# Optimization experiments

Measured on AMD Instinct MI355X. Metric: run time of the kernel, lower is better.

Reference implementation:

```python
import jax, jax.numpy as jnp
import numpy as np
import math

PHI = (1.0 + math.sqrt(5.0)) / 2.0
LUT_SIZE = 4096
D_MODEL = 2048
BATCH = 8192
TWO_PI = 2.0 * math.pi


def lut_sin_cos(theta, sin_table, cos_table):
    """LUT-based sin/cos with linear interpolation over [0, 2*pi)."""
    n = sin_table.shape[0]
    pos = jnp.mod(theta, TWO_PI) * (n / TWO_PI)        # [B, D] in [0, n)
    i0f = jnp.floor(pos)
    frac = pos - i0f
    i0 = i0f.astype(jnp.int32) % n
    i1 = (i0 + 1) % n
    s = sin_table[i0] * (1.0 - frac) + sin_table[i1] * frac
    c = cos_table[i0] * (1.0 - frac) + cos_table[i1] * frac
    return s, c


def setup_inputs() -> dict:
    key = jax.random.key(0)
    ks = jax.random.split(key, 6)
    x_real = jax.random.normal(ks[0], (BATCH, D_MODEL), dtype=jnp.float32)
    x_imag = jax.random.normal(ks[1], (BATCH, D_MODEL), dtype=jnp.float32)
    t = jax.random.uniform(ks[2], (BATCH,), dtype=jnp.float32)
    memory_real = jnp.zeros((BATCH, D_MODEL), dtype=jnp.float32)
    memory_imag = jnp.zeros((BATCH, D_MODEL), dtype=jnp.float32)
    w_trigger = jax.random.normal(ks[3], (D_MODEL,), dtype=jnp.float32) * 0.02
    b_trigger = jnp.zeros((D_MODEL,), dtype=jnp.float32)
    w_state = jax.random.normal(ks[4], (D_MODEL,), dtype=jnp.float32) * 0.02
    b_state = jnp.zeros((D_MODEL,), dtype=jnp.float32)
    k = jnp.asarray(3.0, dtype=jnp.float32)
    grid = jnp.arange(LUT_SIZE, dtype=jnp.float32) * (TWO_PI / LUT_SIZE)
    sin_table = jnp.sin(grid)
    cos_table = jnp.cos(grid)
    return dict(x_real=x_real, x_imag=x_imag, t=t,
                memory_real=memory_real, memory_imag=memory_imag,
                w_trigger=w_trigger, b_trigger=b_trigger,
                w_state=w_state, b_state=b_state, k=k,
                sin_table=sin_table, cos_table=cos_table)


def reference(x_real, x_imag, t, memory_real, memory_imag,
              w_trigger, b_trigger, w_state, b_state, k,
              sin_table, cos_table):
    scale = math.sqrt(x_real.shape[-1])
    t_phi = t[:, None] * PHI                                  # [B, 1]

    # trigger phase
    wl_trigger = 1.0 + jnp.abs(w_trigger)
    theta_tr = x_real / wl_trigger + b_trigger + t_phi
    theta_ti = x_imag / wl_trigger + b_trigger + t_phi
    sin_tr, cos_tr = lut_sin_cos(theta_tr, sin_table, cos_table)
    sin_ti, cos_ti = lut_sin_cos(theta_ti, sin_table, cos_table)
    trigger_real = cos_tr * cos_ti - sin_tr * sin_ti
    trigger_imag = cos_tr * sin_ti + sin_tr * cos_ti

    # interference -> exponential decay gate
    interference_raw = jnp.sum(trigger_real * x_real + trigger_imag * x_imag, axis=-1)
    interference_clamped = jnp.clip(interference_raw / scale, -1.0, 1.0)
    x_inv = (1.0 - interference_clamped) / 2.0
    k_eff = jnp.abs(k) + 0.1
    alpha = jnp.exp(-k_eff * x_inv)[:, None]                  # [B, 1]

    # blend with (detached) memory, then re-evolve
    blended_real = alpha * x_real + (1.0 - alpha) * memory_real
    blended_imag = alpha * x_imag + (1.0 - alpha) * memory_imag
    wl_state = 1.0 + jnp.abs(w_state)
    theta_sr = blended_real / wl_state + b_state + t_phi
    theta_si = blended_imag / wl_state + b_state + t_phi
    sin_sr, cos_sr = lut_sin_cos(theta_sr, sin_table, cos_table)
    sin_si, cos_si = lut_sin_cos(theta_si, sin_table, cos_table)
    evolved_real = cos_sr * cos_si - sin_sr * sin_si
    evolved_imag = cos_sr * sin_si + sin_sr * cos_si
    return evolved_real, evolved_imag
```

## Files before the change

### kernel.cpp

```cpp
#include <hip/hip_runtime.h>

#define DMODEL   2048
#define NTHREADS 256
#define ROWS_PER_BLK 4
#define CHUNKS   8

typedef float fx4 __attribute__((ext_vector_type(4)));

__device__ __forceinline__ void fast_sincos(float theta, float& s, float& c) {
    const float INV_TWO_PI = 0.15915494309189535f;
    float r  = theta * INV_TWO_PI;
    float rr = r - floorf(r);
#if __has_builtin(__builtin_amdgcn_sinf) && __has_builtin(__builtin_amdgcn_cosf)
    s = __builtin_amdgcn_sinf(rr);
    c = __builtin_amdgcn_cosf(rr);
#else
    s = __sinf(rr * 6.283185307179586f);
    c = __cosf(rr * 6.283185307179586f);
#endif
}

__device__ __forceinline__ float fast_rcp(float x) {
#if __has_builtin(__builtin_amdgcn_rcpf)
    return __builtin_amdgcn_rcpf(x);
#else
    return 1.0f / x;
#endif
}

template <typename T>
__device__ __forceinline__ void nt_store(T v, T* p) {
#if __has_builtin(__builtin_nontemporal_store)
    __builtin_nontemporal_store(v, p);
#else
    *p = v;
#endif
}

__global__ __launch_bounds__(NTHREADS, 4)
void liquid_echo_kernel(const float* __restrict__ x_real,
                        const float* __restrict__ x_imag,
                        const float* __restrict__ tvec,
                        const float* __restrict__ memory_real,
                        const float* __restrict__ memory_imag,
                        const float* __restrict__ w_trigger,
                        const float* __restrict__ b_trigger,
                        const float* __restrict__ w_state,
                        const float* __restrict__ b_state,
                        const float* __restrict__ kptr,
                        float* __restrict__ out,
                        int nrows,
                        size_t imag_off)
{
    const int lane = threadIdx.x & 63;
    const int row  = blockIdx.x * ROWS_PER_BLK + (threadIdx.x >> 6);
    if (row >= nrows) return;

    const float t_phi = tvec[row] * 1.6180339887498948f;
    const size_t rb   = (size_t)row * DMODEL;
    const int cbase   = lane << 2;

    fx4 xr[CHUNKS], xi[CHUNKS];
    #pragma unroll
    for (int k = 0; k < CHUNKS; ++k) {
        const int c = (k << 8) + cbase;
        xr[k] = *(const fx4*)(x_real + rb + c);
        xi[k] = *(const fx4*)(x_imag + rb + c);
    }

    float sxy[CHUNKS * 4];
    float partial = 0.0f;
    #pragma unroll
    for (int k = 0; k < CHUNKS; ++k) {
        const int c = (k << 8) + cbase;
        const fx4 wt = *(const fx4*)(w_trigger + c);
        const fx4 bt = *(const fx4*)(b_trigger + c);
        #pragma unroll
        for (int j = 0; j < 4; ++j) {
            float iw   = fast_rcp(1.0f + fabsf(wt[j]));
            float base = bt[j] + t_phi;
            float sx   = xr[k][j] + xi[k][j];
            sxy[k * 4 + j] = sx;
            float ths  = fmaf(sx, iw, base + base);
            float s, cc;
            fast_sincos(ths, s, cc);
            partial = fmaf(cc, xr[k][j], partial);
            partial = fmaf(s,  xi[k][j], partial);
        }
    }

    fx4 mr[CHUNKS], mi[CHUNKS];
    #pragma unroll
    for (int k = 0; k < CHUNKS; ++k) {
        const int c = (k << 8) + cbase;
        mr[k] = *(const fx4*)(memory_real + rb + c);
        mi[k] = *(const fx4*)(memory_imag + rb + c);
    }

    #pragma unroll
    for (int off = 32; off > 0; off >>= 1)
        partial += __shfl_xor(partial, off, 64);

    float ic    = partial * (1.0f / 45.254833995939045f);
    ic          = fminf(1.0f, fmaxf(-1.0f, ic));
    float x_inv = (1.0f - ic) * 0.5f;
    float k_eff = fabsf(kptr[0]) + 0.1f;
    const float alpha = __expf(-k_eff * x_inv);
    const float oma   = 1.0f - alpha;

    float* outr = out + rb;
    float* outi = out + imag_off + rb;

    #pragma unroll
    for (int k = 0; k < CHUNKS; ++k) {
        const int c = (k << 8) + cbase;
        const fx4 ws = *(const fx4*)(w_state + c);
        const fx4 bs = *(const fx4*)(b_state + c);
        fx4 er, ei;
        #pragma unroll
        for (int j = 0; j < 4; ++j) {
            float smm  = mr[k][j] + mi[k][j];
            float sb   = fmaf(alpha, sxy[k * 4 + j], oma * smm);
            float iw   = fast_rcp(1.0f + fabsf(ws[j]));
            float base = bs[j] + t_phi;
            float ths  = fmaf(sb, iw, base + base);
            float s, cc;
            fast_sincos(ths, s, cc);
            er[j] = cc;
            ei[j] = s;
        }
        nt_store(er, (fx4*)(outr + c));
        nt_store(ei, (fx4*)(outi + c));
    }
}

extern "C" void kernel_launch(void* const* d_in, const int* in_sizes, int n_in,
                              void* d_out, int out_size, void* d_ws, size_t ws_size,
                              hipStream_t stream) {
    const float* x_real      = (const float*)d_in[0];
    const float* x_imag      = (const float*)d_in[1];
    const float* t           = (const float*)d_in[2];
    const float* memory_real = (const float*)d_in[3];
    const float* memory_imag = (const float*)d_in[4];
    const float* w_trigger   = (const float*)d_in[5];
    const float* b_trigger   = (const float*)d_in[6];
    const float* w_state     = (const float*)d_in[7];
    const float* b_state     = (const float*)d_in[8];
    const float* k           = (const float*)d_in[9];
    float* out = (float*)d_out;

    int B = in_sizes[0] / DMODEL;
    size_t imag_off = (size_t)out_size / 2;
    int grid = (B + ROWS_PER_BLK - 1) / ROWS_PER_BLK;

    liquid_echo_kernel<<<grid, NTHREADS, 0, stream>>>(
        x_real, x_imag, t, memory_real, memory_imag,
        w_trigger, b_trigger, w_state, b_state, k,
        out, B, imag_off);
}
```

Measured before the change: 346.2 us.

## Split into interference-reduction kernel and grid-stride double-buffered evolve kernel

```diff
diff --git a/kernel.cpp b/kernel.cpp
--- a/kernel.cpp
+++ b/kernel.cpp
@@ -1,11 +1,16 @@
 #include <hip/hip_runtime.h>
 
-#define DMODEL   2048
-#define NTHREADS 256
-#define ROWS_PER_BLK 4
-#define CHUNKS   8
+#define DMODEL    2048
+#define F4ROW     (DMODEL / 4)
+#define ROWSHIFT  9
+#define NTHREADS  256
+#define WPB       (NTHREADS / 64)
+#define MAXBLK    2048
+#define MAXROWS_STATIC 16384
 
 typedef float fx4 __attribute__((ext_vector_type(4)));
+
+__device__ float g_rowsum[MAXROWS_STATIC];
 
 __device__ __forceinline__ void fast_sincos(float theta, float& s, float& c) {
     const float INV_TWO_PI = 0.15915494309189535f;
@@ -37,101 +42,139 @@
 #endif
 }
 
-__global__ __launch_bounds__(NTHREADS, 4)
-void liquid_echo_kernel(const float* __restrict__ x_real,
-                        const float* __restrict__ x_imag,
-                        const float* __restrict__ tvec,
-                        const float* __restrict__ memory_real,
-                        const float* __restrict__ memory_imag,
-                        const float* __restrict__ w_trigger,
-                        const float* __restrict__ b_trigger,
-                        const float* __restrict__ w_state,
-                        const float* __restrict__ b_state,
-                        const float* __restrict__ kptr,
-                        float* __restrict__ out,
-                        int nrows,
-                        size_t imag_off)
+__global__ __launch_bounds__(NTHREADS)
+void k1_interference(const float* __restrict__ x_real,
+                     const float* __restrict__ x_imag,
+                     const float* __restrict__ tvec,
+                     const float* __restrict__ w_trigger,
+                     const float* __restrict__ b_trigger,
+                     float* __restrict__ rowsum_ext,
+                     int use_ext,
+                     int nrows)
 {
     const int lane = threadIdx.x & 63;
-    const int row  = blockIdx.x * ROWS_PER_BLK + (threadIdx.x >> 6);
+    const int row  = blockIdx.x * WPB + (threadIdx.x >> 6);
     if (row >= nrows) return;
 
+    float* __restrict__ rowsum = use_ext ? rowsum_ext : g_rowsum;
+
     const float t_phi = tvec[row] * 1.6180339887498948f;
-    const size_t rb   = (size_t)row * DMODEL;
-    const int cbase   = lane << 2;
-
-    fx4 xr[CHUNKS], xi[CHUNKS];
+    const fx4* Xr = (const fx4*)x_real + (size_t)row * F4ROW;
+    const fx4* Xi = (const fx4*)x_imag + (size_t)row * F4ROW;
+    const fx4* Wt = (const fx4*)w_trigger;
+    const fx4* Bt = (const fx4*)b_trigger;
+
+    float p = 0.0f;
     #pragma unroll
-    for (int k = 0; k < CHUNKS; ++k) {
-        const int c = (k << 8) + cbase;
-        xr[k] = *(const fx4*)(x_real + rb + c);
-        xi[k] = *(const fx4*)(x_imag + rb + c);
-    }
-
-    float sxy[CHUNKS * 4];
-    float partial = 0.0f;
-    #pragma unroll
-    for (int k = 0; k < CHUNKS; ++k) {
-        const int c = (k << 8) + cbase;
-        const fx4 wt = *(const fx4*)(w_trigger + c);
-        const fx4 bt = *(const fx4*)(b_trigger + c);
+    for (int k = 0; k < 8; ++k) {
+        const int c = k * 64 + lane;
+        const fx4 xr = Xr[c];
+        const fx4 xi = Xi[c];
+        const fx4 wt = Wt[c];
+        const fx4 bt = Bt[c];
         #pragma unroll
         for (int j = 0; j < 4; ++j) {
             float iw   = fast_rcp(1.0f + fabsf(wt[j]));
             float base = bt[j] + t_phi;
-            float sx   = xr[k][j] + xi[k][j];
-            sxy[k * 4 + j] = sx;
-            float ths  = fmaf(sx, iw, base + base);
             float s, cc;
-            fast_sincos(ths, s, cc);
-            partial = fmaf(cc, xr[k][j], partial);
-            partial = fmaf(s,  xi[k][j], partial);
+            fast_sincos(fmaf(xr[j] + xi[j], iw, base + base), s, cc);
+            p = fmaf(cc, xr[j], p);
+            p = fmaf(s,  xi[j], p);
         }
     }
-
-    fx4 mr[CHUNKS], mi[CHUNKS];
-    #pragma unroll
-    for (int k = 0; k < CHUNKS; ++k) {
-        const int c = (k << 8) + cbase;
-        mr[k] = *(const fx4*)(memory_real + rb + c);
-        mi[k] = *(const fx4*)(memory_imag + rb + c);
-    }
-
     #pragma unroll
     for (int off = 32; off > 0; off >>= 1)
-        partial += __shfl_xor(partial, off, 64);
-
-    float ic    = partial * (1.0f / 45.254833995939045f);
+        p += __shfl_xor(p, off, 64);
+    if (lane == 0) rowsum[row] = p;
+}
+
+
+struct S2 { fx4 xr, xi, mr, mi, ws, bs; float tphi, sum; };
+
+__device__ __forceinline__ void load2(S2& S, int g,
+        const float* __restrict__ xr, const float* __restrict__ xi,
+        const float* __restrict__ mr, const float* __restrict__ mi,
+        const float* __restrict__ tv, const float* __restrict__ rowsum,
+        const float* __restrict__ ws, const float* __restrict__ bs) {
+    S.xr = ((const fx4*)xr)[g];
+    S.xi = ((const fx4*)xi)[g];
+    S.mr = ((const fx4*)mr)[g];
+    S.mi = ((const fx4*)mi)[g];
+    const int c = g & (F4ROW - 1);
+    S.ws = ((const fx4*)ws)[c];
+    S.bs = ((const fx4*)bs)[c];
+    const int row = g >> ROWSHIFT;
+    S.tphi = tv[row] * 1.6180339887498948f;
+    S.sum  = rowsum[row];
+}
+
+__device__ __forceinline__ void compute2(const S2& S, int g, float k_eff,
+                                         float* __restrict__ outr,
+                                         float* __restrict__ outi) {
+    float ic    = S.sum * (1.0f / 45.254833995939045f);
     ic          = fminf(1.0f, fmaxf(-1.0f, ic));
     float x_inv = (1.0f - ic) * 0.5f;
-    float k_eff = fabsf(kptr[0]) + 0.1f;
     const float alpha = __expf(-k_eff * x_inv);
     const float oma   = 1.0f - alpha;
-
-    float* outr = out + rb;
-    float* outi = out + imag_off + rb;
-
+    fx4 er, ei;
     #pragma unroll
-    for (int k = 0; k < CHUNKS; ++k) {
-        const int c = (k << 8) + cbase;
-        const fx4 ws = *(const fx4*)(w_state + c);
-        const fx4 bs = *(const fx4*)(b_state + c);
-        fx4 er, ei;
-        #pragma unroll
-        for (int j = 0; j < 4; ++j) {
-            float smm  = mr[k][j] + mi[k][j];
-            float sb   = fmaf(alpha, sxy[k * 4 + j], oma * smm);
-            float iw   = fast_rcp(1.0f + fabsf(ws[j]));
-            float base = bs[j] + t_phi;
-            float ths  = fmaf(sb, iw, base + base);
-            float s, cc;
-            fast_sincos(ths, s, cc);
-            er[j] = cc;
-            ei[j] = s;
+    for (int j = 0; j < 4; ++j) {
+        float sb   = fmaf(alpha, S.xr[j] + S.xi[j], oma * (S.mr[j] + S.mi[j]));
+        float iw   = fast_rcp(1.0f + fabsf(S.ws[j]));
+        float base = S.bs[j] + S.tphi;
+        float s, c;
+        fast_sincos(fmaf(sb, iw, base + base), s, c);
+        er[j] = c;
+        ei[j] = s;
+    }
+    nt_store(er, (fx4*)outr + g);
+    nt_store(ei, (fx4*)outi + g);
+}
+
+__global__ __launch_bounds__(NTHREADS)
+void k2_evolve(const float* __restrict__ x_real,
+               const float* __restrict__ x_imag,
+               const float* __restrict__ tvec,
+               const float* __restrict__ memory_real,
+               const float* __restrict__ memory_imag,
+               const float* __restrict__ w_state,
+               const float* __restrict__ b_state,
+               const float* __restrict__ kptr,
+               const float* __restrict__ rowsum_ext,
+               int use_ext,
+               float* __restrict__ out,
+               int n_f4,
+               size_t imag_off)
+{
+    const float* __restrict__ rowsum = use_ext ? rowsum_ext : g_rowsum;
+    const float k_eff = fabsf(kptr[0]) + 0.1f;
+    float* outr = out;
+    float* outi = out + imag_off;
+
+    const int stride = gridDim.x * blockDim.x;
+    int g = blockIdx.x * blockDim.x + threadIdx.x;
+    if (g >= n_f4) return;
+
+    S2 A, B;
+    load2(A, g, x_real, x_imag, memory_real, memory_imag,
+          tvec, rowsum, w_state, b_state);
+    int gn = g + stride;
+    while (gn < n_f4) {
+        load2(B, gn, x_real, x_imag, memory_real, memory_imag,
+              tvec, rowsum, w_state, b_state);
+        compute2(A, g, k_eff, outr, outi);
+        g = gn; gn += stride;
+        if (gn < n_f4) {
+            load2(A, gn, x_real, x_imag, memory_real, memory_imag,
+                  tvec, rowsum, w_state, b_state);
+            compute2(B, g, k_eff, outr, outi);
+            g = gn; gn += stride;
+        } else {
+            compute2(B, g, k_eff, outr, outi);
+            return;
         }
-        nt_store(er, (fx4*)(outr + c));
-        nt_store(ei, (fx4*)(outi + c));
     }
+    compute2(A, g, k_eff, outr, outi);
 }
 
 extern "C" void kernel_launch(void* const* d_in, const int* in_sizes, int n_in,
@@ -149,12 +192,22 @@
     const float* k           = (const float*)d_in[9];
     float* out = (float*)d_out;
 
-    int B = in_sizes[0] / DMODEL;
-    size_t imag_off = (size_t)out_size / 2;
-    int grid = (B + ROWS_PER_BLK - 1) / ROWS_PER_BLK;
-
-    liquid_echo_kernel<<<grid, NTHREADS, 0, stream>>>(
+    const int B    = in_sizes[0] / DMODEL;
+    const int n_f4 = B * F4ROW;
+    const size_t imag_off = (size_t)out_size / 2;
+
+    const int use_ext = (B > MAXROWS_STATIC &&
+                         ws_size >= (size_t)B * sizeof(float)) ? 1 : 0;
+    float* rowsum_ext = (float*)d_ws;
+
+    int grid1 = (B + WPB - 1) / WPB;
+    int grid2 = (n_f4 + NTHREADS - 1) / NTHREADS;
+    if (grid2 > MAXBLK) grid2 = MAXBLK;
+
+    k1_interference<<<grid1, NTHREADS, 0, stream>>>(
+        x_real, x_imag, t, w_trigger, b_trigger, rowsum_ext, use_ext, B);
+
+    k2_evolve<<<grid2, NTHREADS, 0, stream>>>(
         x_real, x_imag, t, memory_real, memory_imag,
-        w_trigger, b_trigger, w_state, b_state, k,
-        out, B, imag_off);
-}
+        w_state, b_state, k, rowsum_ext, use_ext, out, n_f4, imag_off);
+}
```

Result: no change. 350.4 us (+1.2%).
